# Kernel tuning notes

Measured on AMD Instinct MI355X. Metric: run time of the kernel, lower is better.

Reference implementation:

```python
import jax, jax.numpy as jnp
import numpy as np

B, T, D, H, HORIZON, OUT = 1024, 64, 128, 128, 24, 1
ATT = 64  # attention MLP hidden size


def _p(key, shape, scale=0.05):
    return scale * jax.random.normal(key, shape, dtype=jnp.float32)


def setup_inputs() -> dict:
    ks = jax.random.split(jax.random.key(0), 20)
    return dict(
        X=jax.random.normal(ks[0], (B, T, D), jnp.float32),
        y_hist=jax.random.normal(ks[1], (B, T), jnp.float32),
        We_w=_p(ks[2], (ATT, 2 * H + 1)), We_b=_p(ks[3], (ATT,)),
        ve_w=_p(ks[4], (1, ATT)), ve_b=_p(ks[5], (1,)),
        enc_Wih=_p(ks[6], (4 * H, D)), enc_Whh=_p(ks[7], (4 * H, H)),
        enc_bih=_p(ks[8], (4 * H,)), enc_bhh=_p(ks[9], (4 * H,)),
        dec_Wih=_p(ks[10], (4 * H, 1)), dec_Whh=_p(ks[11], (4 * H, H)),
        dec_bih=_p(ks[12], (4 * H,)), dec_bhh=_p(ks[13], (4 * H,)),
        Wd_w=_p(ks[14], (ATT, 3 * H)), Wd_b=_p(ks[15], (ATT,)),
        vd_w=_p(ks[16], (1, ATT)), vd_b=_p(ks[17], (1,)),
        fc_w=_p(ks[18], (OUT, 2 * H + T)), fc_b=_p(ks[19], (OUT,)),
    )


def _lstm_cell(x, h, c, Wih, Whh, bih, bhh):
    # torch.nn.LSTMCell gate order: i, f, g, o
    gates = x @ Wih.T + bih + h @ Whh.T + bhh
    i, f, g, o = jnp.split(gates, 4, axis=1)
    c2 = jax.nn.sigmoid(f) * c + jax.nn.sigmoid(i) * jnp.tanh(g)
    h2 = jax.nn.sigmoid(o) * jnp.tanh(c2)
    return h2, c2


def _forward(X, y_hist, We_w, We_b, ve_w, ve_b,
             enc_Wih, enc_Whh, enc_bih, enc_bhh,
             dec_Wih, dec_Whh, dec_bih, dec_bhh,
             Wd_w, Wd_b, vd_w, vd_b, fc_w, fc_b):
    batch = X.shape[0]
    # --- encoder with input attention (vectorized over the per-k python loop) ---
    W_hs = We_w[:, :2 * H]       # weights on [h_prev, s_prev]
    w_feat = We_w[:, 2 * H]      # weight on the scalar feature, shape (ATT,)

    def enc_step(carry, x_t):
        h, c = carry
        base = jnp.concatenate([h, c], axis=1) @ W_hs.T + We_b        # (B, ATT)
        energy = jnp.tanh(base[:, None, :] + x_t[:, :, None] * w_feat)  # (B, D, ATT)
        scores = energy @ ve_w[0] + ve_b[0]                            # (B, D)
        alpha = jax.nn.softmax(scores, axis=1)
        x_tilde = alpha * x_t
        h2, c2 = _lstm_cell(x_tilde, h, c, enc_Wih, enc_Whh, enc_bih, enc_bhh)
        return (h2, c2), h2

    h0 = jnp.zeros((batch, H), X.dtype)
    c0 = jnp.zeros((batch, H), X.dtype)
    _, enc_h = jax.lax.scan(enc_step, (h0, c0), X.transpose(1, 0, 2))
    enc_hiddens = enc_h.transpose(1, 0, 2)  # (B, T, H)

    # --- decoder with temporal attention ---
    # Wd_w columns ordered as cat([encoder_hiddens, d_prev, c_prev])
    enc_proj = jnp.einsum('bth,kh->btk', enc_hiddens, Wd_w[:, :H])  # (B, T, ATT)
    Wd_d, Wd_c = Wd_w[:, H:2 * H], Wd_w[:, 2 * H:]

    def dec_step(carry, _):
        d, cc, y_prev = carry
        dc = d @ Wd_d.T + cc @ Wd_c.T + Wd_b                # (B, ATT)
        energy = jnp.tanh(enc_proj + dc[:, None, :])         # (B, T, ATT)
        score = energy @ vd_w[0] + vd_b[0]                   # (B, T)
        beta = jax.nn.softmax(score, axis=1)
        context = jnp.einsum('bt,bth->bh', beta, enc_hiddens)  # (B, H)
        d2, cc2 = _lstm_cell(y_prev, d, cc, dec_Wih, dec_Whh, dec_bih, dec_bhh)
        fc_in = jnp.concatenate([d2, context, y_hist], axis=1)  # (B, 2H+T)
        out = fc_in @ fc_w.T + fc_b                              # (B, 1)
        return (d2, cc2, out), out

    d0 = jnp.zeros((batch, H), X.dtype)
    cd0 = jnp.zeros((batch, H), X.dtype)
    y0 = y_hist[:, -1:]
    _, outs = jax.lax.scan(dec_step, (d0, cd0, y0), None, length=HORIZON)
    return outs.transpose(1, 0, 2)  # (B, horizon, output_dim)


def reference(X, y_hist, We_w, We_b, ve_w, ve_b,
              enc_Wih, enc_Whh, enc_bih, enc_bhh,
              dec_Wih, dec_Whh, dec_bih, dec_bhh,
              Wd_w, Wd_b, vd_w, vd_b, fc_w, fc_b):
    return _forward(X, y_hist, We_w, We_b, ve_w, ve_b,
                    enc_Wih, enc_Whh, enc_bih, enc_bhh,
                    dec_Wih, dec_Whh, dec_bih, dec_bhh,
                    Wd_w, Wd_b, vd_w, vd_b, fc_w, fc_b)
```

## Files before the change

kernel.cpp:

```cpp
#include <hip/hip_runtime.h>
#include <hip/hip_bf16.h>


#define B_    1024
#define T_    64
#define D_    128
#define H_    128
#define HOR_  24
#define ATT_  64
#define BB    4
#define LOG2E 1.4426950408889634f
#define C127  (1.f/127.f)
#define KLAG  8.245856315e-05f

typedef float f32x4  __attribute__((ext_vector_type(4)));
typedef short bf16x8 __attribute__((ext_vector_type(8)));
typedef int   i32x4  __attribute__((ext_vector_type(4)));

#define MFMA16(a,b,c) __builtin_amdgcn_mfma_f32_16x16x32_bf16((a),(b),(c),0,0,0)
#define MFMAI8(a,b,c) __builtin_amdgcn_mfma_i32_16x16x64_i8((a),(b),(c),0,0,0)

#define WHS_E    0
#define WDDC_E   16384
#define WDENC_E  32768
#define WENC8_B  81920
#define WDEC8_B  212992
#define SENC_B   278528
#define SDEC_B   280576

__device__ __forceinline__ short f2b(float f) {
  union { float f; unsigned u; } c; c.f = f;
  unsigned r = c.u + 0x7fffu + ((c.u >> 16) & 1u);
  return (short)(r >> 16);
}
__device__ __forceinline__ float b2f(short s) {
  union { unsigned u; float f; } c; c.u = ((unsigned)(unsigned short)s) << 16;
  return c.f;
}
__device__ __forceinline__ float fexp2(float x) { return __builtin_amdgcn_exp2f(x); }
__device__ __forceinline__ float frcp (float x) { return __builtin_amdgcn_rcpf(x); }
__device__ __forceinline__ float tanh_acc(float x) {
  float e = fexp2(x * 2.885390081777927f);
  return 1.f - 2.f * frcp(1.f + e);
}
__device__ __forceinline__ float sigm(float x) {
  return frcp(1.f + fexp2(-LOG2E * x));
}

template<int CTRL>
__device__ __forceinline__ float dppmov(float v) {
  return __builtin_bit_cast(float,
      __builtin_amdgcn_mov_dpp(__builtin_bit_cast(int, v), CTRL, 0xF, 0xF, true));
}
__device__ __forceinline__ float swz16(float v) {
  return __builtin_bit_cast(float,
      __builtin_amdgcn_ds_swizzle(__builtin_bit_cast(int, v), 0x401F));
}
__device__ __forceinline__ float wsum64(float v) {
  v += dppmov<0xB1>(v);
  v += dppmov<0x4E>(v);
  v += dppmov<0x141>(v);
  v += dppmov<0x140>(v);
  v += swz16(v);
  v += __shfl_xor(v, 32, 64);
  return v;
}
__device__ __forceinline__ float wmax64(float v) {
  v = fmaxf(v, dppmov<0xB1>(v));
  v = fmaxf(v, dppmov<0x4E>(v));
  v = fmaxf(v, dppmov<0x141>(v));
  v = fmaxf(v, dppmov<0x140>(v));
  v = fmaxf(v, swz16(v));
  v = fmaxf(v, __shfl_xor(v, 32, 64));
  return v;
}
__device__ __forceinline__ float gsum8(float v) {
  v += dppmov<0xB1>(v);
  v += dppmov<0x4E>(v);
  v += dppmov<0x141>(v);
  return v;
}

__global__ void prep_bf(const float* __restrict__ We_w,
                        const float* __restrict__ Wd_w,
                        char* __restrict__ ws8) {
  int e = blockIdx.x * 256 + threadIdx.x;
  if (e >= 40960) return;
  short* f16 = (short*)ws8;
  int region = e >> 14;
  int er = e & 16383;
  int fi = er >> 9, li = (er >> 3) & 63, jq = er & 7;
  int kt = fi >> 2, nt = fi & 3;
  int k = kt * 32 + ((li >> 4) << 3) + jq, n = nt * 16 + (li & 15);
  float v;
  if (region == 0)      v = We_w[n * 257 + k];
  else if (region == 1) v = (k < 128) ? Wd_w[n * 384 + 128 + k]
                                      : Wd_w[n * 384 + 256 + (k - 128)];
  else                  v = Wd_w[n * 384 + k];
  f16[e] = f2b(v);
}

__global__ void prep_q(const float* __restrict__ enc_Wih,
                       const float* __restrict__ enc_Whh,
                       const float* __restrict__ dec_Whh,
                       char* __restrict__ ws8) {
  int gw = (blockIdx.x * 256 + threadIdx.x) >> 6;
  int lane = threadIdx.x & 63;
  if (gw < 512) {
    int n = gw;
    float v[4]; float m = 0.f;
#pragma unroll
    for (int q = 0; q < 4; ++q) {
      int k = lane * 4 + q;
      v[q] = (k < 128) ? enc_Wih[n * 128 + k] : enc_Whh[n * 128 + (k - 128)];
      m = fmaxf(m, fabsf(v[q]));
    }
    m = wmax64(m);
    if (lane == 0) ((float*)(ws8 + SENC_B))[n] = m * C127;
    float inv = m > 0.f ? 127.f / m : 0.f;
    char* dst = ws8 + WENC8_B;
#pragma unroll
    for (int q = 0; q < 4; ++q) {
      int k = lane * 4 + q;
      int kt = k >> 6, grp = (k >> 4) & 3, b = k & 15, l16 = (n & 15) | (grp << 4);
      dst[((kt * 32 + (n >> 4)) * 64 + l16) * 16 + b] = (char)(int)rintf(v[q] * inv);
    }
  } else if (gw < 1024) {
    int n = gw - 512;
    float v[2]; float m = 0.f;
#pragma unroll
    for (int q = 0; q < 2; ++q) {
      int k = lane * 2 + q;
      v[q] = dec_Whh[n * 128 + k];
      m = fmaxf(m, fabsf(v[q]));
    }
    m = wmax64(m);
    if (lane == 0) ((float*)(ws8 + SDEC_B))[n] = m * C127;
    float inv = m > 0.f ? 127.f / m : 0.f;
    char* dst = ws8 + WDEC8_B;
#pragma unroll
    for (int q = 0; q < 2; ++q) {
      int k = lane * 2 + q;
      int kt = k >> 6, grp = (k >> 4) & 3, b = k & 15, l16 = (n & 15) | (grp << 4);
      dst[((kt * 32 + (n >> 4)) * 64 + l16) * 16 + b] = (char)(int)rintf(v[q] * inv);
    }
  }
}

__global__ __launch_bounds__(512, 2)
void da_rnn(const float* __restrict__ X, const float* __restrict__ y_hist,
            const float* __restrict__ We_w, const float* __restrict__ We_b,
            const float* __restrict__ ve_w,
            const float* __restrict__ enc_bih, const float* __restrict__ enc_bhh,
            const float* __restrict__ dec_Wih,
            const float* __restrict__ dec_bih, const float* __restrict__ dec_bhh,
            const float* __restrict__ Wd_b, const float* __restrict__ vd_w,
            const float* __restrict__ fc_w, const float* __restrict__ fc_b,
            const char* __restrict__ ws8, float* __restrict__ out) {
  const short* f16  = (const short*)ws8;
  const i32x4* enc8 = (const i32x4*)(ws8 + WENC8_B);
  const i32x4* dec8 = (const i32x4*)(ws8 + WDEC8_B);
  const float* senc = (const float*)(ws8 + SENC_B);
  const float* sdec = (const float*)(ws8 + SDEC_B);

  __shared__ __align__(16) char  s_A8[16][272];
  __shared__ __align__(16) short s_Ahc[16][264];
  __shared__ short s_projT[4][64][65];
  __shared__ short s_encht[4][128][66];
  __shared__ __align__(16) float s_gates[4][528];
  __shared__ __align__(16) float s_base[4][72];
  __shared__ float s_beta[4][64];
  __shared__ float s_xr[4];
  __shared__ float2 s_wv[64];
  __shared__ __align__(16) float s_web[64];
  __shared__ float s_vd[64];
  __shared__ __align__(16) float s_wdb[64];
  __shared__ float s_se[512], s_sd[512];
  __shared__ float s_encb[512], s_decb[512], s_dwih[512];
  __shared__ float s_fcw[320];

  const int tid  = threadIdx.x;
  const int lane = tid & 63;
  const int w    = tid >> 6;
  const int b0   = blockIdx.x * BB;

  if (tid < 64) {
    s_wv[tid]  = make_float2(We_w[tid * 257 + 256], ve_w[tid]);
    s_web[tid] = We_b[tid];
    s_vd[tid]  = vd_w[tid];
    s_wdb[tid] = Wd_b[tid];
  }
  if (tid < 320) s_fcw[tid] = fc_w[tid];
  s_se[tid]   = senc[tid];
  s_sd[tid]   = sdec[tid];
  s_encb[tid] = enc_bih[tid] + enc_bhh[tid];
  s_decb[tid] = dec_bih[tid] + dec_bhh[tid];
  s_dwih[tid] = dec_Wih[tid];
  for (int i = tid; i < (16 * 272) / 4; i += 512) ((int*)s_A8)[i] = 0;
  for (int i = tid; i < (16 * 264) / 2; i += 512) ((int*)s_Ahc)[i] = 0;
  if (tid < 256) s_base[tid >> 6][tid & 63] = We_b[tid & 63];

  i32x4 wg[4][4];
#pragma unroll
  for (int kt = 0; kt < 4; ++kt)
#pragma unroll
    for (int i = 0; i < 4; ++i)
      wg[kt][i] = enc8[(kt * 32 + (w + 8 * i)) * 64 + lane];
  bf16x8 wb[8], wp[4];
  if (w < 4) {
#pragma unroll
    for (int kt = 0; kt < 8; ++kt)
      wb[kt] = *(const bf16x8*)(f16 + WHS_E + ((kt * 4 + w) * 64 + lane) * 8);
  } else {
#pragma unroll
    for (int kt = 0; kt < 4; ++kt)
      wp[kt] = *(const bf16x8*)(f16 + WDENC_E + ((kt * 4 + (w - 4)) * 64 + lane) * 8);
  }

  float xf0 = 0.f, xf1 = 0.f, xi = 0.f;
  const float* Xr = X + (size_t)(b0 + (w & 3)) * T_ * D_;
  if (w < 4) {
    xf0 = Xr[lane]; xf1 = Xr[64 + lane];
    xi = 6.f * cosf((2 * (lane >> 3) + 1) * 0.19634954084936207f);
  }
  float cM = 0.f;
  const int bM   = lane >> 4;
  const int phil = lane & 15;
  const int phig = (w << 4) + phil;
  i32x4 ahp[4];
#pragma unroll
  for (int i = 0; i < 4; ++i) ahp[i] = (i32x4){0, 0, 0, 0};
  __syncthreads();

  float seM[4], ebM[4];
#pragma unroll
  for (int q = 0; q < 4; ++q) {
    seM[q] = s_se[q * 128 + phig];
    ebM[q] = s_encb[q * 128 + phig];
  }
  f32x4 webq = {0.f, 0.f, 0.f, 0.f};
  if (w < 4) webq = *(const f32x4*)&s_web[(w << 4) + ((lane >> 4) << 2)];

  for (int t = 0; t < T_; ++t) {
    float x0, x1;
    if (w < 4) {
      __builtin_amdgcn_s_setprio(1);
      x0 = xf0; x1 = xf1;
      const int kc = lane & 7;
      float p = 0.f;
      const float4* wvp = (const float4*)&s_wv[kc * 8];
      const float4* bp  = (const float4*)&s_base[w][kc * 8];
      float4 bA = bp[0], bB = bp[1];
#pragma unroll
      for (int q = 0; q < 4; ++q) {
        float4 wv = wvp[q];
        float bb0 = (q < 2) ? ((q & 1) ? bA.z : bA.x) : ((q & 1) ? bB.z : bB.x);
        float bb1 = (q < 2) ? ((q & 1) ? bA.w : bA.y) : ((q & 1) ? bB.w : bB.y);
        p += wv.y * tanh_acc(fmaf(xi, wv.x, bb0));
        p += wv.w * tanh_acc(fmaf(xi, wv.z, bb1));
      }
      p = gsum8(p);
      float f0 = __shfl(p,  0, 64), f1 = __shfl(p,  8, 64);
      float f2 = __shfl(p, 16, 64), f3 = __shfl(p, 24, 64);
      float f4 = __shfl(p, 32, 64), f5 = __shfl(p, 40, 64);
      float f6 = __shfl(p, 48, 64), f7 = __shfl(p, 56, 64);
      float e0, e1;
      {
        const float xb[8] = { 5.884711682f, 4.988817674f, 3.333421398f, 1.170541932f,
                             -1.170541932f, -3.333421398f, -4.988817674f, -5.884711682f};
        const float wbar[8] = { 0.1950903220f, -0.5555702330f, 0.8314696123f, -0.9807852804f,
                                0.9807852804f, -0.8314696123f, 0.5555702330f, -0.1950903220f};
        float fw[8] = {f0 * wbar[0], f1 * wbar[1], f2 * wbar[2], f3 * wbar[3],
                       f4 * wbar[4], f5 * wbar[5], f6 * wbar[6], f7 * wbar[7]};
        float u0 = fminf(fmaxf(x0, -6.f), 6.f), u1 = fminf(fmaxf(x1, -6.f), 6.f);
        float d0[8], d1[8], P0[8], P1[8];
        float pre0 = 1.f, pre1 = 1.f;
#pragma unroll
        for (int i = 0; i < 8; ++i) {
          d0[i] = u0 - xb[i]; d1[i] = u1 - xb[i];
          P0[i] = pre0;       P1[i] = pre1;
          pre0 *= d0[i];      pre1 *= d1[i];
        }
        float suf0 = 1.f, suf1 = 1.f, acc0 = 0.f, acc1 = 0.f;
#pragma unroll
        for (int i = 7; i >= 0; --i) {
          acc0 = fmaf(fw[i] * P0[i], suf0, acc0);
          acc1 = fmaf(fw[i] * P1[i], suf1, acc1);
          suf0 *= d0[i];
          suf1 *= d1[i];
        }
        e0 = fexp2(acc0 * KLAG);
        e1 = fexp2(acc1 * KLAG);
      }
      float sum = wsum64(e0 + e1);
      float mx  = wmax64(fmaxf(e0 * fabsf(x0), e1 * fabsf(x1)));
      float inv = mx > 0.f ? 127.f * frcp(mx) : 0.f;
      s_A8[w][lane]      = (char)(int)rintf(x0 * e0 * inv);
      s_A8[w][64 + lane] = (char)(int)rintf(x1 * e1 * inv);
      if (lane == 0) s_xr[w] = mx * frcp(127.f * sum);
      __builtin_amdgcn_s_setprio(0);
    } else if (t > 0) {
      f32x4 acc = {0.f, 0.f, 0.f, 0.f};
#pragma unroll
      for (int kt = 0; kt < 4; ++kt) {
        bf16x8 a = *(const bf16x8*)&s_Ahc[lane & 15][kt * 32 + ((lane >> 4) << 3)];
        acc = MFMA16(a, wp[kt], acc);
      }
      if (lane < 16) {
        int katt = (w - 4) * 16 + lane;
#pragma unroll
        for (int r = 0; r < 4; ++r) s_projT[r][katt][t - 1] = f2b(acc[r]);
      }
    }
    __syncthreads();
    {
      i32x4 a0 = *(const i32x4*)&s_A8[lane & 15][  0 + ((lane >> 4) << 4)];
      i32x4 a1 = *(const i32x4*)&s_A8[lane & 15][ 64 + ((lane >> 4) << 4)];
      i32x4 ax[4];
#pragma unroll
      for (int i = 0; i < 4; ++i) {
        i32x4 z = {0, 0, 0, 0};
        ax[i] = MFMAI8(wg[1][i], a1, MFMAI8(wg[0][i], a0, z));
      }
      float* scr = ((float*)s_gates) + w * 264;
      float sx = s_xr[lane & 3];
      if ((lane & 15) < 4) {
        int off = ((lane & 15) << 4) + ((lane >> 4) << 2);
#pragma unroll
        for (int i = 0; i < 4; ++i) {
          f32x4 v;
#pragma unroll
          for (int r = 0; r < 4; ++r)
            v[r] = fmaf(sx, (float)ax[i][r], C127 * (float)ahp[i][r]);
          *(f32x4*)&scr[i * 64 + off] = v;
        }
      }
      asm volatile("" ::: "memory");
      int ra = (bM << 4) + phil;
      float g_i = fmaf(scr[      ra], seM[0], ebM[0]);
      float g_f = fmaf(scr[ 64 + ra], seM[1], ebM[1]);
      float g_g = fmaf(scr[128 + ra], seM[2], ebM[2]);
      float g_o = fmaf(scr[192 + ra], seM[3], ebM[3]);
      cM = sigm(g_f) * cM + sigm(g_i) * tanh_acc(g_g);
      float h = sigm(g_o) * tanh_acc(cM);
      s_Ahc[bM][phig]       = f2b(h);
      s_Ahc[bM][128 + phig] = f2b(cM);
      s_A8[bM][128 + phig]  = (char)(int)rintf(h * 127.f);
      s_encht[bM][phig][t]  = f2b(h);
    }
    __syncthreads();
    {
      i32x4 pa2 = *(const i32x4*)&s_A8[lane & 15][128 + ((lane >> 4) << 4)];
      i32x4 pa3 = *(const i32x4*)&s_A8[lane & 15][192 + ((lane >> 4) << 4)];
#pragma unroll
      for (int i = 0; i < 4; ++i) {
        i32x4 z = {0, 0, 0, 0};
        ahp[i] = MFMAI8(wg[3][i], pa3, MFMAI8(wg[2][i], pa2, z));
      }
    }
    if (w < 4) {
      if (t < T_ - 1) {
        xf0 = Xr[(t + 1) * D_ + lane];
        xf1 = Xr[(t + 1) * D_ + 64 + lane];
      }
      f32x4 acc = {0.f, 0.f, 0.f, 0.f}, acc2 = {0.f, 0.f, 0.f, 0.f};
#pragma unroll
      for (int kt = 0; kt < 4; ++kt) {
        bf16x8 a = *(const bf16x8*)&s_Ahc[lane & 15][kt * 32 + ((lane >> 4) << 3)];
        acc = MFMA16(wb[kt], a, acc);
      }
#pragma unroll
      for (int kt = 4; kt < 8; ++kt) {
        bf16x8 a = *(const bf16x8*)&s_Ahc[lane & 15][kt * 32 + ((lane >> 4) << 3)];
        acc2 = MFMA16(wb[kt], a, acc2);
      }
      if ((lane & 15) < 4) {
        f32x4 v = acc + acc2 + webq;
        *(f32x4*)&s_base[lane & 15][(w << 4) + ((lane >> 4) << 2)] = v;
      }
    }
    __syncthreads();
  }
  if (w >= 4) {
    f32x4 acc = {0.f, 0.f, 0.f, 0.f};
#pragma unroll
    for (int kt = 0; kt < 4; ++kt) {
      bf16x8 a = *(const bf16x8*)&s_Ahc[lane & 15][kt * 32 + ((lane >> 4) << 3)];
      acc = MFMA16(a, wp[kt], acc);
    }
    if (lane < 16) {
      int katt = (w - 4) * 16 + lane;
#pragma unroll
      for (int r = 0; r < 4; ++r) s_projT[r][katt][T_ - 1] = f2b(acc[r]);
    }
  }
  __syncthreads();

  {
    int r = tid >> 7, j = tid & 127;
    s_Ahc[r][j] = 0; s_Ahc[r][128 + j] = 0; s_A8[r][j] = 0;
  }
  i32x4 wdg[2][8];
  bf16x8 wdc[8];
  float yp = 0.f, yhd = 0.f;
  float sdC_p[8], db_p[8], dw_p[8];
  f32x4 wdbq = {0.f, 0.f, 0.f, 0.f};
  if (w >= 4) {
#pragma unroll
    for (int kt = 0; kt < 2; ++kt)
#pragma unroll
      for (int i = 0; i < 8; ++i)
        wdg[kt][i] = dec8[(kt * 32 + ((w - 4) * 8 + i)) * 64 + lane];
  } else {
#pragma unroll
    for (int kt = 0; kt < 8; ++kt)
      wdc[kt] = *(const bf16x8*)(f16 + WDDC_E + ((kt * 4 + w) * 64 + lane) * 8);
#pragma unroll
    for (int j = 0; j < 8; ++j) {
      sdC_p[j] = s_sd[lane + 64 * j] * C127;
      db_p[j]  = s_decb[lane + 64 * j];
      dw_p[j]  = s_dwih[lane + 64 * j];
    }
    wdbq = *(const f32x4*)&s_wdb[(w << 4) + ((lane >> 4) << 2)];
    yp = y_hist[(b0 + w) * T_ + (T_ - 1)];
    float pp = s_fcw[256 + lane] * y_hist[(b0 + w) * T_ + lane];
    yhd = wsum64(pp) + fc_b[0];
  }
  float dd0 = 0.f, dc0 = 0.f, dd1 = 0.f, dc1 = 0.f;
  __syncthreads();

  for (int hs = 0; hs < HOR_; ++hs) {
    if (w >= 4) {
      i32x4 a0 = *(const i32x4*)&s_A8[lane & 15][ 0 + ((lane >> 4) << 4)];
      i32x4 a1 = *(const i32x4*)&s_A8[lane & 15][64 + ((lane >> 4) << 4)];
#pragma unroll
      for (int i = 0; i < 8; ++i) {
        i32x4 z = {0, 0, 0, 0};
        i32x4 ac = MFMAI8(wdg[1][i], a1, MFMAI8(wdg[0][i], a0, z));
        if ((lane & 15) < 4) {
          f32x4 v = {(float)ac[0], (float)ac[1], (float)ac[2], (float)ac[3]};
          *(f32x4*)&s_gates[lane & 15][(((w - 4) * 8 + i) << 4) + ((lane >> 4) << 2)] = v;
        }
      }
    } else {
      if (hs > 0) {
        float cx0a = 0.f, cx0b = 0.f, cx1a = 0.f, cx1b = 0.f;
        const short* e0p = &s_encht[w][lane][0];
        const short* e1p = &s_encht[w][lane + 64][0];
#pragma unroll 8
        for (int tp = 0; tp < 32; ++tp) {
          float2 bta = *(const float2*)&s_beta[w][2 * tp];
          short2 h0v = *(const short2*)&e0p[2 * tp];
          short2 h1v = *(const short2*)&e1p[2 * tp];
          cx0a = fmaf(bta.x, b2f(h0v.x), cx0a); cx0b = fmaf(bta.y, b2f(h0v.y), cx0b);
          cx1a = fmaf(bta.x, b2f(h1v.x), cx1a); cx1b = fmaf(bta.y, b2f(h1v.y), cx1b);
        }
        float cx0 = cx0a + cx0b, cx1 = cx1a + cx1b;
        float pf = s_fcw[lane] * dd0 + s_fcw[64 + lane] * dd1
                 + s_fcw[128 + lane] * cx0 + s_fcw[192 + lane] * cx1;
        pf = wsum64(pf);
        float o = pf + yhd;
        if (lane == 0) out[(b0 + w) * HOR_ + (hs - 1)] = o;
        yp = o;
      }
      f32x4 acc = {0.f, 0.f, 0.f, 0.f}, acc2 = {0.f, 0.f, 0.f, 0.f};
#pragma unroll
      for (int kt = 0; kt < 4; ++kt) {
        bf16x8 a = *(const bf16x8*)&s_Ahc[lane & 15][kt * 32 + ((lane >> 4) << 3)];
        acc = MFMA16(wdc[kt], a, acc);
      }
#pragma unroll
      for (int kt = 4; kt < 8; ++kt) {
        bf16x8 a = *(const bf16x8*)&s_Ahc[lane & 15][kt * 32 + ((lane >> 4) << 3)];
        acc2 = MFMA16(wdc[kt], a, acc2);
      }
      if ((lane & 15) < 4) {
        f32x4 v = acc + acc2 + wdbq;
        *(f32x4*)&s_base[lane & 15][(w << 4) + ((lane >> 4) << 2)] = v;
      }
    }
    __syncthreads();
    if (w < 4) {
      float gi0 = s_gates[w][lane]       * sdC_p[0] + db_p[0] + yp * dw_p[0];
      float gi1 = s_gates[w][lane + 64]  * sdC_p[1] + db_p[1] + yp * dw_p[1];
      float gf0 = s_gates[w][lane + 128] * sdC_p[2] + db_p[2] + yp * dw_p[2];
      float gf1 = s_gates[w][lane + 192] * sdC_p[3] + db_p[3] + yp * dw_p[3];
      float gg0 = s_gates[w][lane + 256] * sdC_p[4] + db_p[4] + yp * dw_p[4];
      float gg1 = s_gates[w][lane + 320] * sdC_p[5] + db_p[5] + yp * dw_p[5];
      float go0 = s_gates[w][lane + 384] * sdC_p[6] + db_p[6] + yp * dw_p[6];
      float go1 = s_gates[w][lane + 448] * sdC_p[7] + db_p[7] + yp * dw_p[7];
      dc0 = sigm(gf0) * dc0 + sigm(gi0) * tanh_acc(gg0);
      dd0 = sigm(go0) * tanh_acc(dc0);
      dc1 = sigm(gf1) * dc1 + sigm(gi1) * tanh_acc(gg1);
      dd1 = sigm(go1) * tanh_acc(dc1);
      s_Ahc[w][lane]       = f2b(dd0);
      s_Ahc[w][lane + 64]  = f2b(dd1);
      s_Ahc[w][lane + 128] = f2b(dc0);
      s_Ahc[w][lane + 192] = f2b(dc1);
      s_A8[w][lane]      = (char)(int)rintf(dd0 * 127.f);
      s_A8[w][lane + 64] = (char)(int)rintf(dd1 * 127.f);
    } else {
      __builtin_amdgcn_s_setprio(1);
      const int r = w - 4;
      float sA = 0.f, sB = 0.f, sC = 0.f, sD = 0.f;
#pragma unroll 4
      for (int k = 0; k < 64; k += 4) {
        sA += s_vd[k]     * tanh_acc(b2f(s_projT[r][k][lane])     + s_base[r][k]);
        sB += s_vd[k + 1] * tanh_acc(b2f(s_projT[r][k + 1][lane]) + s_base[r][k + 1]);
        sC += s_vd[k + 2] * tanh_acc(b2f(s_projT[r][k + 2][lane]) + s_base[r][k + 2]);
        sD += s_vd[k + 3] * tanh_acc(b2f(s_projT[r][k + 3][lane]) + s_base[r][k + 3]);
      }
      float s = (sA + sB) + (sC + sD);
      float e = fexp2(s * LOG2E);
      float ssum = wsum64(e);
      s_beta[r][lane] = e * frcp(ssum);
      __builtin_amdgcn_s_setprio(0);
    }
    __syncthreads();
  }
  if (w < 4) {
    float cx0a = 0.f, cx0b = 0.f, cx1a = 0.f, cx1b = 0.f;
    const short* e0p = &s_encht[w][lane][0];
    const short* e1p = &s_encht[w][lane + 64][0];
#pragma unroll 8
    for (int tp = 0; tp < 32; ++tp) {
      float2 bta = *(const float2*)&s_beta[w][2 * tp];
      short2 h0v = *(const short2*)&e0p[2 * tp];
      short2 h1v = *(const short2*)&e1p[2 * tp];
      cx0a = fmaf(bta.x, b2f(h0v.x), cx0a); cx0b = fmaf(bta.y, b2f(h0v.y), cx0b);
      cx1a = fmaf(bta.x, b2f(h1v.x), cx1a); cx1b = fmaf(bta.y, b2f(h1v.y), cx1b);
    }
    float cx0 = cx0a + cx0b, cx1 = cx1a + cx1b;
    float pf = s_fcw[lane] * dd0 + s_fcw[64 + lane] * dd1
             + s_fcw[128 + lane] * cx0 + s_fcw[192 + lane] * cx1;
    pf = wsum64(pf);
    float o = pf + yhd;
    if (lane == 0) out[(b0 + w) * HOR_ + (HOR_ - 1)] = o;
  }
}

extern "C" void kernel_launch(void* const* d_in, const int* in_sizes, int n_in,
                              void* d_out, int out_size, void* d_ws, size_t ws_size,
                              hipStream_t stream) {
  (void)in_sizes; (void)n_in; (void)out_size; (void)ws_size;
  const float* X       = (const float*)d_in[0];
  const float* y_hist  = (const float*)d_in[1];
  const float* We_w    = (const float*)d_in[2];
  const float* We_b    = (const float*)d_in[3];
  const float* ve_w    = (const float*)d_in[4];
  const float* enc_Wih = (const float*)d_in[6];
  const float* enc_Whh = (const float*)d_in[7];
  const float* enc_bih = (const float*)d_in[8];
  const float* enc_bhh = (const float*)d_in[9];
  const float* dec_Wih = (const float*)d_in[10];
  const float* dec_Whh = (const float*)d_in[11];
  const float* dec_bih = (const float*)d_in[12];
  const float* dec_bhh = (const float*)d_in[13];
  const float* Wd_w    = (const float*)d_in[14];
  const float* Wd_b    = (const float*)d_in[15];
  const float* vd_w    = (const float*)d_in[16];
  const float* fc_w    = (const float*)d_in[18];
  const float* fc_b    = (const float*)d_in[19];

  char* ws8  = (char*)d_ws;
  float* out = (float*)d_out;

  prep_bf<<<160, 256, 0, stream>>>(We_w, Wd_w, ws8);
  prep_q <<<256, 256, 0, stream>>>(enc_Wih, enc_Whh, dec_Whh, ws8);
  da_rnn <<<B_ / BB, 512, 0, stream>>>(X, y_hist, We_w, We_b, ve_w,
                                       enc_bih, enc_bhh, dec_Wih, dec_bih, dec_bhh,
                                       Wd_b, vd_w, fc_w, fc_b, ws8, out);
}
```

Before: 294.9 us.

## Template kernel on batch rows per block and launch two-row variant when occupancy allows

The main kernel becomes a template on the number of batch rows per 512-thread block (2 or 4), with shared arrays and guards sized to match and launch bounds asking for 4 blocks per CU in the 2-row case. The host queries occupancy and launches the 2-row variant on 512 blocks if at least two fit per CU, otherwise it keeps the 4-row layout. This doubles the grid so more CUs stay busy on the latency-bound recurrence, at the cost of more padded MFMA work per row and duplicated weight register loads. The encoder attention math is also lightly rearranged to reuse differences inline.

```diff
diff --git a/kernel.cpp b/kernel.cpp
--- a/kernel.cpp
+++ b/kernel.cpp
@@ -8,7 +8,6 @@
 #define H_    128
 #define HOR_  24
 #define ATT_  64
-#define BB    4
 #define LOG2E 1.4426950408889634f
 #define C127  (1.f/127.f)
 #define KLAG  8.245856315e-05f
@@ -147,30 +146,34 @@
   }
 }
 
-__global__ __launch_bounds__(512, 2)
-void da_rnn(const float* __restrict__ X, const float* __restrict__ y_hist,
-            const float* __restrict__ We_w, const float* __restrict__ We_b,
-            const float* __restrict__ ve_w,
-            const float* __restrict__ enc_bih, const float* __restrict__ enc_bhh,
-            const float* __restrict__ dec_Wih,
-            const float* __restrict__ dec_bih, const float* __restrict__ dec_bhh,
-            const float* __restrict__ Wd_b, const float* __restrict__ vd_w,
-            const float* __restrict__ fc_w, const float* __restrict__ fc_b,
-            const char* __restrict__ ws8, float* __restrict__ out) {
+template<int NB>
+__global__ __launch_bounds__(512, (NB == 2 ? 4 : 2))
+void da_rnn_t(const float* __restrict__ X, const float* __restrict__ y_hist,
+              const float* __restrict__ We_w, const float* __restrict__ We_b,
+              const float* __restrict__ ve_w,
+              const float* __restrict__ enc_bih, const float* __restrict__ enc_bhh,
+              const float* __restrict__ dec_Wih,
+              const float* __restrict__ dec_bih, const float* __restrict__ dec_bhh,
+              const float* __restrict__ Wd_b, const float* __restrict__ vd_w,
+              const float* __restrict__ fc_w, const float* __restrict__ fc_b,
+              const char* __restrict__ ws8, float* __restrict__ out) {
   const short* f16  = (const short*)ws8;
   const i32x4* enc8 = (const i32x4*)(ws8 + WENC8_B);
   const i32x4* dec8 = (const i32x4*)(ws8 + WDEC8_B);
   const float* senc = (const float*)(ws8 + SENC_B);
   const float* sdec = (const float*)(ws8 + SDEC_B);
 
+  constexpr int SCR_PW = (NB == 4) ? 264 : 132;
+  constexpr int SCR_G  = (NB == 4) ? 64  : 32;
+
   __shared__ __align__(16) char  s_A8[16][272];
   __shared__ __align__(16) short s_Ahc[16][264];
-  __shared__ short s_projT[4][64][65];
-  __shared__ short s_encht[4][128][66];
-  __shared__ __align__(16) float s_gates[4][528];
-  __shared__ __align__(16) float s_base[4][72];
-  __shared__ float s_beta[4][64];
-  __shared__ float s_xr[4];
+  __shared__ short s_projT[NB][64][65];
+  __shared__ short s_encht[NB][128][66];
+  __shared__ __align__(16) float s_gates[NB][528];
+  __shared__ __align__(16) float s_base[NB][72];
+  __shared__ float s_beta[NB][64];
+  __shared__ float s_xr[NB];
   __shared__ float2 s_wv[64];
   __shared__ __align__(16) float s_web[64];
   __shared__ float s_vd[64];
@@ -182,7 +185,7 @@
   const int tid  = threadIdx.x;
   const int lane = tid & 63;
   const int w    = tid >> 6;
-  const int b0   = blockIdx.x * BB;
+  const int b0   = blockIdx.x * NB;
 
   if (tid < 64) {
     s_wv[tid]  = make_float2(We_w[tid * 257 + 256], ve_w[tid]);
@@ -198,7 +201,7 @@
   s_dwih[tid] = dec_Wih[tid];
   for (int i = tid; i < (16 * 272) / 4; i += 512) ((int*)s_A8)[i] = 0;
   for (int i = tid; i < (16 * 264) / 2; i += 512) ((int*)s_Ahc)[i] = 0;
-  if (tid < 256) s_base[tid >> 6][tid & 63] = We_b[tid & 63];
+  if (tid < 64 * NB) s_base[tid >> 6][tid & 63] = We_b[tid & 63];
 
   i32x4 wg[4][4];
 #pragma unroll
@@ -218,8 +221,8 @@
   }
 
   float xf0 = 0.f, xf1 = 0.f, xi = 0.f;
-  const float* Xr = X + (size_t)(b0 + (w & 3)) * T_ * D_;
-  if (w < 4) {
+  const float* Xr = X + (size_t)(b0 + (w & (NB - 1))) * T_ * D_;
+  if (w < NB) {
     xf0 = Xr[lane]; xf1 = Xr[64 + lane];
     xi = 6.f * cosf((2 * (lane >> 3) + 1) * 0.19634954084936207f);
   }
@@ -243,7 +246,7 @@
 
   for (int t = 0; t < T_; ++t) {
     float x0, x1;
-    if (w < 4) {
+    if (w < NB) {
       __builtin_amdgcn_s_setprio(1);
       x0 = xf0; x1 = xf1;
       const int kc = lane & 7;
@@ -260,34 +263,32 @@
         p += wv.w * tanh_acc(fmaf(xi, wv.z, bb1));
       }
       p = gsum8(p);
-      float f0 = __shfl(p,  0, 64), f1 = __shfl(p,  8, 64);
-      float f2 = __shfl(p, 16, 64), f3 = __shfl(p, 24, 64);
-      float f4 = __shfl(p, 32, 64), f5 = __shfl(p, 40, 64);
-      float f6 = __shfl(p, 48, 64), f7 = __shfl(p, 56, 64);
+      float fv0 = __shfl(p,  0, 64), fv1 = __shfl(p,  8, 64);
+      float fv2 = __shfl(p, 16, 64), fv3 = __shfl(p, 24, 64);
+      float fv4 = __shfl(p, 32, 64), fv5 = __shfl(p, 40, 64);
+      float fv6 = __shfl(p, 48, 64), fv7 = __shfl(p, 56, 64);
       float e0, e1;
       {
         const float xb[8] = { 5.884711682f, 4.988817674f, 3.333421398f, 1.170541932f,
                              -1.170541932f, -3.333421398f, -4.988817674f, -5.884711682f};
         const float wbar[8] = { 0.1950903220f, -0.5555702330f, 0.8314696123f, -0.9807852804f,
                                 0.9807852804f, -0.8314696123f, 0.5555702330f, -0.1950903220f};
-        float fw[8] = {f0 * wbar[0], f1 * wbar[1], f2 * wbar[2], f3 * wbar[3],
-                       f4 * wbar[4], f5 * wbar[5], f6 * wbar[6], f7 * wbar[7]};
+        float fvv[8] = {fv0, fv1, fv2, fv3, fv4, fv5, fv6, fv7};
         float u0 = fminf(fmaxf(x0, -6.f), 6.f), u1 = fminf(fmaxf(x1, -6.f), 6.f);
-        float d0[8], d1[8], P0[8], P1[8];
+        float P0[8], P1[8];
         float pre0 = 1.f, pre1 = 1.f;
 #pragma unroll
         for (int i = 0; i < 8; ++i) {
-          d0[i] = u0 - xb[i]; d1[i] = u1 - xb[i];
-          P0[i] = pre0;       P1[i] = pre1;
-          pre0 *= d0[i];      pre1 *= d1[i];
+          P0[i] = pre0;            P1[i] = pre1;
+          pre0 *= (u0 - xb[i]);    pre1 *= (u1 - xb[i]);
         }
         float suf0 = 1.f, suf1 = 1.f, acc0 = 0.f, acc1 = 0.f;
 #pragma unroll
         for (int i = 7; i >= 0; --i) {
-          acc0 = fmaf(fw[i] * P0[i], suf0, acc0);
-          acc1 = fmaf(fw[i] * P1[i], suf1, acc1);
-          suf0 *= d0[i];
-          suf1 *= d1[i];
+          acc0 = fmaf(fvv[i] * (wbar[i] * P0[i]), suf0, acc0);
+          acc1 = fmaf(fvv[i] * (wbar[i] * P1[i]), suf1, acc1);
+          suf0 *= (u0 - xb[i]);
+          suf1 *= (u1 - xb[i]);
         }
         e0 = fexp2(acc0 * KLAG);
         e1 = fexp2(acc1 * KLAG);
@@ -299,7 +300,7 @@
       s_A8[w][64 + lane] = (char)(int)rintf(x1 * e1 * inv);
       if (lane == 0) s_xr[w] = mx * frcp(127.f * sum);
       __builtin_amdgcn_s_setprio(0);
-    } else if (t > 0) {
+    } else if (w >= 4 && t > 0) {
       f32x4 acc = {0.f, 0.f, 0.f, 0.f};
 #pragma unroll
       for (int kt = 0; kt < 4; ++kt) {
@@ -309,7 +310,7 @@
       if (lane < 16) {
         int katt = (w - 4) * 16 + lane;
 #pragma unroll
-        for (int r = 0; r < 4; ++r) s_projT[r][katt][t - 1] = f2b(acc[r]);
+        for (int r = 0; r < NB; ++r) s_projT[r][katt][t - 1] = f2b(acc[r]);
       }
     }
     __syncthreads();
@@ -322,9 +323,9 @@
         i32x4 z = {0, 0, 0, 0};
         ax[i] = MFMAI8(wg[1][i], a1, MFMAI8(wg[0][i], a0, z));
       }
-      float* scr = ((float*)s_gates) + w * 264;
-      float sx = s_xr[lane & 3];
-      if ((lane & 15) < 4) {
+      float* scr = ((float*)s_gates) + w * SCR_PW;
+      float sx = s_xr[lane & (NB - 1)];
+      if ((lane & 15) < NB) {
         int off = ((lane & 15) << 4) + ((lane >> 4) << 2);
 #pragma unroll
         for (int i = 0; i < 4; ++i) {
@@ -332,21 +333,23 @@
 #pragma unroll
           for (int r = 0; r < 4; ++r)
             v[r] = fmaf(sx, (float)ax[i][r], C127 * (float)ahp[i][r]);
-          *(f32x4*)&scr[i * 64 + off] = v;
+          *(f32x4*)&scr[i * SCR_G + off] = v;
         }
       }
       asm volatile("" ::: "memory");
-      int ra = (bM << 4) + phil;
-      float g_i = fmaf(scr[      ra], seM[0], ebM[0]);
-      float g_f = fmaf(scr[ 64 + ra], seM[1], ebM[1]);
-      float g_g = fmaf(scr[128 + ra], seM[2], ebM[2]);
-      float g_o = fmaf(scr[192 + ra], seM[3], ebM[3]);
-      cM = sigm(g_f) * cM + sigm(g_i) * tanh_acc(g_g);
-      float h = sigm(g_o) * tanh_acc(cM);
-      s_Ahc[bM][phig]       = f2b(h);
-      s_Ahc[bM][128 + phig] = f2b(cM);
-      s_A8[bM][128 + phig]  = (char)(int)rintf(h * 127.f);
-      s_encht[bM][phig][t]  = f2b(h);
+      if (bM < NB) {
+        int ra = (bM << 4) + phil;
+        float g_i = fmaf(scr[0 * SCR_G + ra], seM[0], ebM[0]);
+        float g_f = fmaf(scr[1 * SCR_G + ra], seM[1], ebM[1]);
+        float g_g = fmaf(scr[2 * SCR_G + ra], seM[2], ebM[2]);
+        float g_o = fmaf(scr[3 * SCR_G + ra], seM[3], ebM[3]);
+        cM = sigm(g_f) * cM + sigm(g_i) * tanh_acc(g_g);
+        float h = sigm(g_o) * tanh_acc(cM);
+        s_Ahc[bM][phig]       = f2b(h);
+        s_Ahc[bM][128 + phig] = f2b(cM);
+        s_A8[bM][128 + phig]  = (char)(int)rintf(h * 127.f);
+        s_encht[bM][phig][t]  = f2b(h);
+      }
     }
     __syncthreads();
     {
@@ -358,11 +361,11 @@
         ahp[i] = MFMAI8(wg[3][i], pa3, MFMAI8(wg[2][i], pa2, z));
       }
     }
+    if (w < NB && t < T_ - 1) {
+      xf0 = Xr[(t + 1) * D_ + lane];
+      xf1 = Xr[(t + 1) * D_ + 64 + lane];
+    }
     if (w < 4) {
-      if (t < T_ - 1) {
-        xf0 = Xr[(t + 1) * D_ + lane];
-        xf1 = Xr[(t + 1) * D_ + 64 + lane];
-      }
       f32x4 acc = {0.f, 0.f, 0.f, 0.f}, acc2 = {0.f, 0.f, 0.f, 0.f};
 #pragma unroll
       for (int kt = 0; kt < 4; ++kt) {
@@ -374,7 +377,7 @@
         bf16x8 a = *(const bf16x8*)&s_Ahc[lane & 15][kt * 32 + ((lane >> 4) << 3)];
         acc2 = MFMA16(wb[kt], a, acc2);
       }
-      if ((lane & 15) < 4) {
+      if ((lane & 15) < NB) {
         f32x4 v = acc + acc2 + webq;
         *(f32x4*)&s_base[lane & 15][(w << 4) + ((lane >> 4) << 2)] = v;
       }
@@ -391,14 +394,14 @@
     if (lane < 16) {
       int katt = (w - 4) * 16 + lane;
 #pragma unroll
-      for (int r = 0; r < 4; ++r) s_projT[r][katt][T_ - 1] = f2b(acc[r]);
+      for (int r = 0; r < NB; ++r) s_projT[r][katt][T_ - 1] = f2b(acc[r]);
     }
   }
   __syncthreads();
 
   {
     int r = tid >> 7, j = tid & 127;
-    s_Ahc[r][j] = 0; s_Ahc[r][128 + j] = 0; s_A8[r][j] = 0;
+    if (r < NB) { s_Ahc[r][j] = 0; s_Ahc[r][128 + j] = 0; s_A8[r][j] = 0; }
   }
   i32x4 wdg[2][8];
   bf16x8 wdc[8];
@@ -415,16 +418,18 @@
 #pragma unroll
     for (int kt = 0; kt < 8; ++kt)
       wdc[kt] = *(const bf16x8*)(f16 + WDDC_E + ((kt * 4 + w) * 64 + lane) * 8);
-#pragma unroll
-    for (int j = 0; j < 8; ++j) {
-      sdC_p[j] = s_sd[lane + 64 * j] * C127;
-      db_p[j]  = s_decb[lane + 64 * j];
-      dw_p[j]  = s_dwih[lane + 64 * j];
-    }
     wdbq = *(const f32x4*)&s_wdb[(w << 4) + ((lane >> 4) << 2)];
-    yp = y_hist[(b0 + w) * T_ + (T_ - 1)];
-    float pp = s_fcw[256 + lane] * y_hist[(b0 + w) * T_ + lane];
-    yhd = wsum64(pp) + fc_b[0];
+    if (w < NB) {
+#pragma unroll
+      for (int j = 0; j < 8; ++j) {
+        sdC_p[j] = s_sd[lane + 64 * j] * C127;
+        db_p[j]  = s_decb[lane + 64 * j];
+        dw_p[j]  = s_dwih[lane + 64 * j];
+      }
+      yp = y_hist[(b0 + w) * T_ + (T_ - 1)];
+      float pp = s_fcw[256 + lane] * y_hist[(b0 + w) * T_ + lane];
+      yhd = wsum64(pp) + fc_b[0];
+    }
   }
   float dd0 = 0.f, dc0 = 0.f, dd1 = 0.f, dc1 = 0.f;
   __syncthreads();
@@ -437,13 +442,13 @@
       for (int i = 0; i < 8; ++i) {
         i32x4 z = {0, 0, 0, 0};
         i32x4 ac = MFMAI8(wdg[1][i], a1, MFMAI8(wdg[0][i], a0, z));
-        if ((lane & 15) < 4) {
+        if ((lane & 15) < NB) {
           f32x4 v = {(float)ac[0], (float)ac[1], (float)ac[2], (float)ac[3]};
           *(f32x4*)&s_gates[lane & 15][(((w - 4) * 8 + i) << 4) + ((lane >> 4) << 2)] = v;
         }
       }
     } else {
-      if (hs > 0) {
+      if (hs > 0 && w < NB) {
         float cx0a = 0.f, cx0b = 0.f, cx1a = 0.f, cx1b = 0.f;
         const short* e0p = &s_encht[w][lane][0];
         const short* e1p = &s_encht[w][lane + 64][0];
@@ -474,13 +479,13 @@
         bf16x8 a = *(const bf16x8*)&s_Ahc[lane & 15][kt * 32 + ((lane >> 4) << 3)];
         acc2 = MFMA16(wdc[kt], a, acc2);
       }
-      if ((lane & 15) < 4) {
+      if ((lane & 15) < NB) {
         f32x4 v = acc + acc2 + wdbq;
         *(f32x4*)&s_base[lane & 15][(w << 4) + ((lane >> 4) << 2)] = v;
       }
     }
     __syncthreads();
-    if (w < 4) {
+    if (w < NB) {
       float gi0 = s_gates[w][lane]       * sdC_p[0] + db_p[0] + yp * dw_p[0];
       float gi1 = s_gates[w][lane + 64]  * sdC_p[1] + db_p[1] + yp * dw_p[1];
       float gf0 = s_gates[w][lane + 128] * sdC_p[2] + db_p[2] + yp * dw_p[2];
@@ -499,7 +504,7 @@
       s_Ahc[w][lane + 192] = f2b(dc1);
       s_A8[w][lane]      = (char)(int)rintf(dd0 * 127.f);
       s_A8[w][lane + 64] = (char)(int)rintf(dd1 * 127.f);
-    } else {
+    } else if (w >= 4 && (w - 4) < NB) {
       __builtin_amdgcn_s_setprio(1);
       const int r = w - 4;
       float sA = 0.f, sB = 0.f, sC = 0.f, sD = 0.f;
@@ -518,7 +523,7 @@
     }
     __syncthreads();
   }
-  if (w < 4) {
+  if (w < NB) {
     float cx0a = 0.f, cx0b = 0.f, cx1a = 0.f, cx1b = 0.f;
     const short* e0p = &s_encht[w][lane][0];
     const short* e1p = &s_encht[w][lane + 64][0];
@@ -567,7 +572,19 @@
 
   prep_bf<<<160, 256, 0, stream>>>(We_w, Wd_w, ws8);
   prep_q <<<256, 256, 0, stream>>>(enc_Wih, enc_Whh, dec_Whh, ws8);
-  da_rnn <<<B_ / BB, 512, 0, stream>>>(X, y_hist, We_w, We_b, ve_w,
-                                       enc_bih, enc_bhh, dec_Wih, dec_bih, dec_bhh,
-                                       Wd_b, vd_w, fc_w, fc_b, ws8, out);
-}
+
+  int nb2 = 0;
+  (void)hipOccupancyMaxActiveBlocksPerMultiprocessor(
+      &nb2, reinterpret_cast<const void*>(&da_rnn_t<2>), 512, 0);
+  if (nb2 >= 2) {
+    da_rnn_t<2><<<B_ / 2, 512, 0, stream>>>(X, y_hist, We_w, We_b, ve_w,
+                                            enc_bih, enc_bhh, dec_Wih, dec_bih,
+                                            dec_bhh, Wd_b, vd_w, fc_w, fc_b,
+                                            ws8, out);
+  } else {
+    da_rnn_t<4><<<B_ / 4, 512, 0, stream>>>(X, y_hist, We_w, We_b, ve_w,
+                                            enc_bih, enc_bhh, dec_Wih, dec_bih,
+                                            dec_bhh, Wd_b, vd_w, fc_w, fc_b,
+                                            ws8, out);
+  }
+}
```

After: 296.7 us. No clear change (+0.6%).
